# Optimization experiments

Hardware: AMD Instinct MI355X
Metric: run time of the kernel (lower is better)

The kernel has to match this reference:

```python
import jax, jax.numpy as jnp
import numpy as np

N_NODES = 50000
N_EDGES = 800000
D_IN = 256
D_OUT = 256
BN_EPS = 1e-5


def setup_inputs() -> dict:
    key = jax.random.key(0)
    ks = jax.random.split(key, 10)
    h = jax.random.normal(ks[0], (N_NODES, D_IN), dtype=jnp.float32)
    e = jax.random.uniform(ks[1], (N_EDGES, 1), dtype=jnp.float32)
    src = jax.random.randint(ks[2], (N_EDGES,), 0, N_NODES, dtype=jnp.int32)
    dst = jax.random.randint(ks[3], (N_EDGES,), 0, N_NODES, dtype=jnp.int32)
    s1 = 1.0 / np.sqrt(D_IN)
    s2 = 1.0 / np.sqrt(D_OUT)
    W1 = jax.random.uniform(ks[4], (D_OUT, D_IN), jnp.float32, -s1, s1)
    b1 = jax.random.uniform(ks[5], (D_OUT,), jnp.float32, -s1, s1)
    W2 = jax.random.uniform(ks[6], (D_OUT, D_OUT), jnp.float32, -s2, s2)
    b2 = jax.random.uniform(ks[7], (D_OUT,), jnp.float32, -s2, s2)
    gamma = jnp.ones((D_OUT,), jnp.float32)
    beta = jnp.zeros((D_OUT,), jnp.float32)
    return {"h": h, "e": e, "src": src, "dst": dst, "W1": W1, "b1": b1,
            "W2": W2, "b2": b2, "gamma": gamma, "beta": beta}


def reference(h, e, src, dst, W1, b1, W2, b2, gamma, beta):
    N = h.shape[0]
    # u_mul_e: gather source node feats, scale by per-edge weight. msg: [E, D_IN]
    msg = h[src] * e
    # mean aggregation over incoming edges per destination node
    agg = jax.ops.segment_sum(msg, dst, num_segments=N)
    deg = jax.ops.segment_sum(jnp.ones((src.shape[0],), h.dtype), dst, num_segments=N)
    hn = jnp.where(deg[:, None] > 0, agg / jnp.maximum(deg, 1.0)[:, None], 0.0)
    # 2-layer MLP with ReLU
    x = jax.nn.relu(hn @ W1.T + b1)
    x = jax.nn.relu(x @ W2.T + b2)
    # BatchNorm1d (training mode: batch statistics, biased variance)
    mu = jnp.mean(x, axis=0)
    var = jnp.var(x, axis=0)
    x = gamma * (x - mu) * jax.lax.rsqrt(var + BN_EPS) + beta
    # residual (in_feats == out_feats): add aggregated features
    return x + hn
```

## Files before the change

### kernel.cpp

```cpp
#include <hip/hip_runtime.h>

#define D 256
#define NCHUNK 512
#define MAXBKT 1024
#define EBCAP 2176

typedef __attribute__((ext_vector_type(8))) short bf16x8;
typedef __attribute__((ext_vector_type(8))) unsigned short u16x8;
typedef __attribute__((ext_vector_type(4))) float f32x4;

__device__ __forceinline__ unsigned short bfr(float x) {
    unsigned u = __float_as_uint(x);
    unsigned r = (u + 0x7fffu + ((u >> 16) & 1u)) >> 16;
    return (unsigned short)r;
}
__device__ __forceinline__ float bf2f(unsigned short u) {
    return __uint_as_float(((unsigned)u) << 16);
}
__device__ __forceinline__ void gload_lds16(const void* g, void* l) {
    __builtin_amdgcn_global_load_lds((const __attribute__((address_space(1))) unsigned int*)g,
                                     (__attribute__((address_space(3))) unsigned int*)l, 16, 0, 0);
}

__global__ void cvt_kernel(const float* __restrict__ in, unsigned short* __restrict__ out,
                           long n4, const float* __restrict__ W1, const float* __restrict__ W2,
                           unsigned short* __restrict__ w1b, unsigned short* __restrict__ w2b) {
    long stride = (long)gridDim.x * blockDim.x;
    long i0 = (long)blockIdx.x * blockDim.x + threadIdx.x;
    for (long i = i0; i < n4; i += stride) {
        float4 v = reinterpret_cast<const float4*>(in)[i];
        ushort4 o;
        o.x = bfr(v.x); o.y = bfr(v.y); o.z = bfr(v.z); o.w = bfr(v.w);
        reinterpret_cast<ushort4*>(out)[i] = o;
    }
    for (long i = i0; i < 16384; i += stride) {
        float4 a = reinterpret_cast<const float4*>(W1)[i];
        float4 b = reinterpret_cast<const float4*>(W2)[i];
        ushort4 oa, ob;
        oa.x = bfr(a.x); oa.y = bfr(a.y); oa.z = bfr(a.z); oa.w = bfr(a.w);
        ob.x = bfr(b.x); ob.y = bfr(b.y); ob.z = bfr(b.z); ob.w = bfr(b.w);
        reinterpret_cast<ushort4*>(w1b)[i] = oa;
        reinterpret_cast<ushort4*>(w2b)[i] = ob;
    }
}

__global__ void bucket_hist_kernel(const int* __restrict__ dst, int* __restrict__ cntA,
                                   int E, int EPC, int nbkt) {
    __shared__ int hist[MAXBKT];
    int c = blockIdx.x, t = threadIdx.x;
    for (int i = t; i < nbkt; i += 256) hist[i] = 0;
    __syncthreads();
    int eend = min(E, (c + 1) * EPC);
    for (int i = c * EPC + t; i < eend; i += 256) atomicAdd(&hist[dst[i] >> 6], 1);
    __syncthreads();
    for (int i = t; i < nbkt; i += 256) cntA[(size_t)c * nbkt + i] = hist[i];
}

__global__ __launch_bounds__(NCHUNK) void bucket_base_kernel(const int* __restrict__ cntA,
                                                             int* __restrict__ relbase,
                                                             int* __restrict__ btot, int nbkt) {
    int b = blockIdx.x, c = threadIdx.x;
    int v = cntA[(size_t)c * nbkt + b];
    int lane = c & 63, w = c >> 6;
    int s = v;
    for (int off = 1; off < 64; off <<= 1) {
        int u = __shfl_up(s, off, 64);
        if (lane >= off) s += u;
    }
    __shared__ int wsum[NCHUNK / 64];
    if (lane == 63) wsum[w] = s;
    __syncthreads();
    int woff = 0;
#pragma unroll
    for (int i = 0; i < NCHUNK / 64; ++i) if (i < w) woff += wsum[i];
    int incl = s + woff;
    relbase[(size_t)c * nbkt + b] = incl - v;
    if (c == NCHUNK - 1) btot[b] = incl;
}

__global__ void bucket_scatter_kernel(const int* __restrict__ src, const float* __restrict__ e,
                                      const int* __restrict__ dst, const int* __restrict__ relbase,
                                      const int* __restrict__ btot, int2* __restrict__ ev,
                                      int E, int EPC, int nbkt) {
    __shared__ int cur[MAXBKT];
    __shared__ int boff[MAXBKT];
    __shared__ int wsum[4];
    int c = blockIdx.x, t = threadIdx.x;
    {
        int base = t * 4;
        int c0 = 0, c1 = 0, c2 = 0, c3 = 0;
        if (base + 3 < nbkt) {
            int4 cc = *reinterpret_cast<const int4*>(&btot[base]);
            c0 = cc.x; c1 = cc.y; c2 = cc.z; c3 = cc.w;
        } else {
            if (base + 0 < nbkt) c0 = btot[base + 0];
            if (base + 1 < nbkt) c1 = btot[base + 1];
            if (base + 2 < nbkt) c2 = btot[base + 2];
            if (base + 3 < nbkt) c3 = btot[base + 3];
        }
        int s0 = c0, s1 = s0 + c1, s2 = s1 + c2, s3 = s2 + c3;
        int lane = t & 63, w = t >> 6;
        int v = s3;
        for (int off = 1; off < 64; off <<= 1) {
            int u = __shfl_up(v, off, 64);
            if (lane >= off) v += u;
        }
        if (lane == 63) wsum[w] = v;
        __syncthreads();
        int woff = 0;
#pragma unroll
        for (int i = 0; i < 4; ++i) if (i < w) woff += wsum[i];
        int p = woff + (v - s3);
        if (base + 0 < nbkt) boff[base + 0] = p;
        if (base + 1 < nbkt) boff[base + 1] = p + s0;
        if (base + 2 < nbkt) boff[base + 2] = p + s1;
        if (base + 3 < nbkt) boff[base + 3] = p + s2;
    }
    __syncthreads();
    for (int i = t; i < nbkt; i += 256) cur[i] = relbase[(size_t)c * nbkt + i] + boff[i];
    __syncthreads();
    int eend = min(E, (c + 1) * EPC);
    for (int i = c * EPC + t; i < eend; i += 256) {
        int d = dst[i];
        int pos = atomicAdd(&cur[d >> 6], 1);
        ev[pos] = make_int2(src[i] | ((d & 63) << 16), __float_as_int(e[i]));
    }
}

__global__ __launch_bounds__(256) void reorder_kernel(const int2* __restrict__ ev,
                                                      const int* __restrict__ btot,
                                                      int* __restrict__ offsets,
                                                      int2* __restrict__ ev2, int N, int nbkt,
                                                      int E) {
    __shared__ int2 ebr[EBCAP];
    __shared__ int2 eb2[EBCAP];
    __shared__ int cnt[64], loff[64], cur[64];
    __shared__ int wsum[4];
    __shared__ int ebeg_s;
    int b = blockIdx.x, t = threadIdx.x;
    int ns = b * 64;
    int nn = min(N, ns + 64) - ns;
    if (t < 64) { cnt[t] = 0; cur[t] = 0; }
    {
        int base = t * 4;
        int c0 = 0, c1 = 0, c2 = 0, c3 = 0;
        if (base + 3 < nbkt) {
            int4 cc = *reinterpret_cast<const int4*>(&btot[base]);
            c0 = cc.x; c1 = cc.y; c2 = cc.z; c3 = cc.w;
        } else {
            if (base + 0 < nbkt) c0 = btot[base + 0];
            if (base + 1 < nbkt) c1 = btot[base + 1];
            if (base + 2 < nbkt) c2 = btot[base + 2];
            if (base + 3 < nbkt) c3 = btot[base + 3];
        }
        int s0 = c0, s1 = s0 + c1, s2 = s1 + c2, s3 = s2 + c3;
        int lane = t & 63, w = t >> 6;
        int v = s3;
        for (int off = 1; off < 64; off <<= 1) {
            int u = __shfl_up(v, off, 64);
            if (lane >= off) v += u;
        }
        if (lane == 63) wsum[w] = v;
        __syncthreads();
        int woff = 0;
#pragma unroll
        for (int i = 0; i < 4; ++i) if (i < w) woff += wsum[i];
        int p = woff + (v - s3);
        if (b >= base && b < base + 4) {
            int pb = p;
            if (b > base + 0) pb += s0 - s0, pb = p + ((b == base + 1) ? s0 : (b == base + 2) ? s1 : s2);
            else pb = p;
            ebeg_s = pb;
        }
    }
    __syncthreads();
    int ebeg = ebeg_s;
    int ecnt = min(btot[b], EBCAP);
    for (int i = t; i < ecnt; i += 256) {
        int2 v = ev[ebeg + i];
        ebr[i] = v;
        atomicAdd(&cnt[(v.x >> 16) & 63], 1);
    }
    __syncthreads();
    if (t < 64) {
        int v = cnt[t];
        int s = v;
        for (int off = 1; off < 64; off <<= 1) {
            int u = __shfl_up(s, off, 64);
            if (t >= off) s += u;
        }
        loff[t] = s - v;
        if (t < nn) offsets[ns + t + 1] = ebeg + s;
    }
    if (b == 0 && t == 0) offsets[0] = 0;
    __syncthreads();
    for (int i = t; i < ecnt; i += 256) {
        int2 v = ebr[i];
        int nl = (v.x >> 16) & 63;
        int p = loff[nl] + atomicAdd(&cur[nl], 1);
        eb2[p] = make_int2(v.x & 0xffff, v.y);
    }
    __syncthreads();
    for (int i = t; i < ecnt; i += 256) ev2[ebeg + i] = eb2[i];
}

__global__ void aggregate_kernel(const unsigned short* __restrict__ hb, const int2* __restrict__ ev,
                                 const int* __restrict__ offsets, unsigned short* __restrict__ hnb,
                                 int n_nodes) {
    int wid = blockIdx.x * 4 + (threadIdx.x >> 6);
    if (wid >= n_nodes) return;
    int lane = threadIdx.x & 63;
    int beg = offsets[wid], end = offsets[wid + 1];
    float ax = 0.f, ay = 0.f, az = 0.f, aw = 0.f;
    int k = beg;
    for (; k + 8 <= end; k += 8) {
        int2 ee[8];
        ushort4 hh[8];
#pragma unroll
        for (int u = 0; u < 8; ++u) ee[u] = ev[k + u];
#pragma unroll
        for (int u = 0; u < 8; ++u)
            hh[u] = *reinterpret_cast<const ushort4*>(&hb[(size_t)ee[u].x * D + lane * 4]);
#pragma unroll
        for (int u = 0; u < 8; ++u) {
            float w0 = __int_as_float(ee[u].y);
            ax += bf2f(hh[u].x) * w0; ay += bf2f(hh[u].y) * w0;
            az += bf2f(hh[u].z) * w0; aw += bf2f(hh[u].w) * w0;
        }
    }
    for (; k < end; ++k) {
        int2 e0 = ev[k];
        ushort4 h0 = *reinterpret_cast<const ushort4*>(&hb[(size_t)e0.x * D + lane * 4]);
        float w0 = __int_as_float(e0.y);
        ax += bf2f(h0.x) * w0; ay += bf2f(h0.y) * w0;
        az += bf2f(h0.z) * w0; aw += bf2f(h0.w) * w0;
    }
    int deg = end - beg;
    float inv = (deg > 0) ? (1.0f / (float)deg) : 0.0f;
    ushort4 o;
    o.x = bfr(ax * inv); o.y = bfr(ay * inv); o.z = bfr(az * inv); o.w = bfr(aw * inv);
    *reinterpret_cast<ushort4*>(&hnb[(size_t)wid * D + lane * 4]) = o;
}

template <int FUSE_STATS>
__global__ __launch_bounds__(256) void gemm_kernel(const unsigned short* __restrict__ A,
                                                   const unsigned short* __restrict__ Wb,
                                                   const float* __restrict__ bias,
                                                   unsigned short* __restrict__ Cout,
                                                   float* __restrict__ partial, int P2, int M) {
    __shared__ short As[128 * 64];
    __shared__ short Bs[128 * 64];
    const int t = threadIdx.x;
    const int row0 = blockIdx.x * 128;
    const int col0 = blockIdx.y * 128;
    const int lane = t & 63;
    const int w = t >> 6;
    const int wr = (w >> 1) * 64;
    const int wc = (w & 1) * 64;
    const int lr = lane & 15;
    const int q = lane >> 4;

    f32x4 zero = {0.f, 0.f, 0.f, 0.f};
    f32x4 acc[4][4];
#pragma unroll
    for (int i = 0; i < 4; ++i)
#pragma unroll
        for (int j = 0; j < 4; ++j) acc[i][j] = zero;

    const char* Ab = reinterpret_cast<const char*>(A);
    const char* Bb = reinterpret_cast<const char*>(Wb);

#pragma unroll
    for (int kt = 0; kt < 4; ++kt) {
#pragma unroll
        for (int i = 0; i < 4; ++i) {
            int g = i * 256 + t;
            int r = g >> 3;
            int so = ((g & 7) << 4) ^ ((r & 7) << 4);
            gload_lds16(Ab + (size_t)(row0 + r) * 512 + kt * 128 + so,
                        reinterpret_cast<char*>(As) + g * 16);
        }
#pragma unroll
        for (int i = 0; i < 4; ++i) {
            int g = i * 256 + t;
            int r = g >> 3;
            int so = ((g & 7) << 4) ^ ((r & 7) << 4);
            gload_lds16(Bb + (size_t)(col0 + r) * 512 + kt * 128 + so,
                        reinterpret_cast<char*>(Bs) + g * 16);
        }
        __syncthreads();
#pragma unroll
        for (int ks = 0; ks < 2; ++ks) {
            bf16x8 a[4], b[4];
#pragma unroll
            for (int fr = 0; fr < 4; ++fr) {
                int r = wr + fr * 16 + lr;
                a[fr] = *reinterpret_cast<const bf16x8*>(
                    reinterpret_cast<const char*>(As) + r * 128 +
                    ((ks * 64 + q * 16) ^ ((r & 7) << 4)));
            }
#pragma unroll
            for (int fc = 0; fc < 4; ++fc) {
                int r = wc + fc * 16 + lr;
                b[fc] = *reinterpret_cast<const bf16x8*>(
                    reinterpret_cast<const char*>(Bs) + r * 128 +
                    ((ks * 64 + q * 16) ^ ((r & 7) << 4)));
            }
#pragma unroll
            for (int fr = 0; fr < 4; ++fr)
#pragma unroll
                for (int fc = 0; fc < 4; ++fc)
                    acc[fr][fc] = __builtin_amdgcn_mfma_f32_16x16x32_bf16(a[fr], b[fc],
                                                                          acc[fr][fc], 0, 0, 0);
        }
        if (kt < 3) __syncthreads();
    }

    float csum[4] = {0.f, 0.f, 0.f, 0.f};
    float csq[4] = {0.f, 0.f, 0.f, 0.f};
#pragma unroll
    for (int fc = 0; fc < 4; ++fc) {
        int col = col0 + wc + fc * 16 + lr;
        float bv = bias[col];
#pragma unroll
        for (int fr = 0; fr < 4; ++fr) {
#pragma unroll
            for (int rr = 0; rr < 4; ++rr) {
                int row = row0 + wr + fr * 16 + q * 4 + rr;
                if (row < M) {
                    float v = fmaxf(acc[fr][fc][rr] + bv, 0.f);
                    Cout[(size_t)row * D + col] = bfr(v);
                    if (FUSE_STATS) { csum[fc] += v; csq[fc] += v * v; }
                }
            }
        }
    }

    if (FUSE_STATS) {
#pragma unroll
        for (int fc = 0; fc < 4; ++fc) {
            float s = csum[fc], qq = csq[fc];
            s += __shfl_xor(s, 16, 64); s += __shfl_xor(s, 32, 64);
            qq += __shfl_xor(qq, 16, 64); qq += __shfl_xor(qq, 32, 64);
            if (lane < 16) {
                int col = col0 + wc + fc * 16 + lane;
                int slot = blockIdx.x * 2 + (w >> 1);
                partial[(size_t)col * P2 + slot] = s;
                partial[(size_t)(col + 256) * P2 + slot] = qq;
            }
        }
    }
}

__global__ void bn_finalize_kernel(const float* __restrict__ partial, const float* __restrict__ gamma,
                                   const float* __restrict__ beta, float* __restrict__ scaleshift,
                                   int nslots, int P2, int n) {
    int c = blockIdx.x;
    int t = threadIdx.x;
    float s = 0.f, q = 0.f;
    for (int b = t; b < nslots; b += 256) {
        s += partial[(size_t)c * P2 + b];
        q += partial[(size_t)(c + 256) * P2 + b];
    }
    int lane = t & 63, w = t >> 6;
    for (int off = 1; off < 64; off <<= 1) {
        s += __shfl_xor(s, off, 64);
        q += __shfl_xor(q, off, 64);
    }
    __shared__ float ss[4], qs[4];
    if (lane == 0) { ss[w] = s; qs[w] = q; }
    __syncthreads();
    if (t == 0) {
        float S = ss[0] + ss[1] + ss[2] + ss[3];
        float Q = qs[0] + qs[1] + qs[2] + qs[3];
        float mu = S / (float)n;
        float var = Q / (float)n - mu * mu;
        float rs = rsqrtf(var + 1e-5f);
        float sc = gamma[c] * rs;
        scaleshift[c] = sc;
        scaleshift[D + c] = beta[c] - mu * sc;
    }
}

__global__ void bn_apply_kernel(float* __restrict__ out, const unsigned short* __restrict__ x2b,
                                const unsigned short* __restrict__ hnb,
                                const float* __restrict__ scaleshift, long total4) {
    long stride = (long)gridDim.x * blockDim.x;
    for (long i = (long)blockIdx.x * blockDim.x + threadIdx.x; i < total4; i += stride) {
        int c4 = (int)(i & 63);
        ushort4 xu = reinterpret_cast<const ushort4*>(x2b)[i];
        ushort4 hu = reinterpret_cast<const ushort4*>(hnb)[i];
        float4 sc = reinterpret_cast<const float4*>(scaleshift)[c4];
        float4 sh = reinterpret_cast<const float4*>(scaleshift)[64 + c4];
        float4 v;
        v.x = bf2f(xu.x) * sc.x + sh.x + bf2f(hu.x);
        v.y = bf2f(xu.y) * sc.y + sh.y + bf2f(hu.y);
        v.z = bf2f(xu.z) * sc.z + sh.z + bf2f(hu.z);
        v.w = bf2f(xu.w) * sc.w + sh.w + bf2f(hu.w);
        reinterpret_cast<float4*>(out)[i] = v;
    }
}

extern "C" void kernel_launch(void* const* d_in, const int* in_sizes, int n_in,
                              void* d_out, int out_size, void* d_ws, size_t ws_size,
                              hipStream_t stream) {
    const float* h     = (const float*)d_in[0];
    const float* e     = (const float*)d_in[1];
    const int*   src   = (const int*)d_in[2];
    const int*   dst   = (const int*)d_in[3];
    const float* W1    = (const float*)d_in[4];
    const float* b1    = (const float*)d_in[5];
    const float* W2    = (const float*)d_in[6];
    const float* b2    = (const float*)d_in[7];
    const float* gamma = (const float*)d_in[8];
    const float* beta  = (const float*)d_in[9];
    float* out = (float*)d_out;

    const int N = in_sizes[0] / D;
    const int E = in_sizes[2];
    const size_t NB = (size_t)N * D;
    const int nrb = (N + 127) / 128;
    const int nslots = nrb * 2;
    const int P2 = (nslots + 15) & ~15;
    const int nbkt = (N + 63) / 64;
    const int EPC = (E + NCHUNK - 1) / NCHUNK;

    char* ws = (char*)d_ws;
    unsigned short* h_bf = (unsigned short*)ws; ws += NB * 2;
    unsigned short* hnb  = (unsigned short*)ws; ws += NB * 2;
    unsigned short* x1b  = (unsigned short*)ws; ws += NB * 2;
    int2* ev             = (int2*)ws;           ws += (size_t)E * 8;
    int2* ev2            = (int2*)ws;           ws += (size_t)E * 8;
    float* partial       = (float*)ws;          ws += (size_t)512 * P2 * 4;
    float* scaleshift    = (float*)ws;          ws += 2 * D * sizeof(float);
    int* offsets         = (int*)ws;            ws += (size_t)(N + 1) * 4;
    int* cntA            = (int*)ws;            ws += (size_t)NCHUNK * nbkt * 4;
    int* relbase         = (int*)ws;            ws += (size_t)NCHUNK * nbkt * 4;
    int* btot            = (int*)ws;            ws += (size_t)nbkt * 4;
    unsigned short* w1b  = (unsigned short*)ws; ws += (size_t)D * D * 2;
    unsigned short* w2b  = (unsigned short*)ws; ws += (size_t)D * D * 2;
    unsigned short* x2b  = h_bf;

    cvt_kernel<<<2048, 256, 0, stream>>>(h, h_bf, (long)(NB / 4), W1, W2, w1b, w2b);

    bucket_hist_kernel<<<NCHUNK, 256, 0, stream>>>(dst, cntA, E, EPC, nbkt);
    bucket_base_kernel<<<nbkt, NCHUNK, 0, stream>>>(cntA, relbase, btot, nbkt);
    bucket_scatter_kernel<<<NCHUNK, 256, 0, stream>>>(src, e, dst, relbase, btot, ev,
                                                      E, EPC, nbkt);
    reorder_kernel<<<nbkt, 256, 0, stream>>>(ev, btot, offsets, ev2, N, nbkt, E);

    aggregate_kernel<<<(N + 3) / 4, 256, 0, stream>>>(h_bf, ev2, offsets, hnb, N);

    dim3 ggrid(nrb, 2);
    gemm_kernel<0><<<ggrid, 256, 0, stream>>>(hnb, w1b, b1, x1b, nullptr, P2, N);
    gemm_kernel<1><<<ggrid, 256, 0, stream>>>(x1b, w2b, b2, x2b, partial, P2, N);

    bn_finalize_kernel<<<256, 256, 0, stream>>>(partial, gamma, beta, scaleshift, nslots, P2, N);
    bn_apply_kernel<<<2048, 256, 0, stream>>>(out, x2b, hnb, scaleshift, (long)(NB / 4));
}
```

Before: 189.3 us.

## Slice aggregation by feature columns and split edges across lane groups

Replaces the one-wave-per-node aggregation with a kernel where each block handles a 64-byte feature slice (8 slices per row), and within a wave 4 groups of 16 lanes process different edges in parallel, reducing with cross-lane shuffles. Adjacent blocks work on the same nodes but different column slices, so the edge list is re-read 8 times, in exchange for more parallelism per node and possibly better cache locality per slice. Each gathered access is now 64 bytes per edge per slice, and the grid is 8x larger.

New measurement: 281.4 us. 1.49x slower.

```diff
diff --git a/kernel.cpp b/kernel.cpp
--- a/kernel.cpp
+++ b/kernel.cpp
@@ -6,7 +6,6 @@
 #define EBCAP 2176
 
 typedef __attribute__((ext_vector_type(8))) short bf16x8;
-typedef __attribute__((ext_vector_type(8))) unsigned short u16x8;
 typedef __attribute__((ext_vector_type(4))) float f32x4;
 
 __device__ __forceinline__ unsigned short bfr(float x) {
@@ -168,7 +167,7 @@
         int p = woff + (v - s3);
         if (b >= base && b < base + 4) {
             int pb = p;
-            if (b > base + 0) pb += s0 - s0, pb = p + ((b == base + 1) ? s0 : (b == base + 2) ? s1 : s2);
+            if (b > base + 0) pb = p + ((b == base + 1) ? s0 : (b == base + 2) ? s1 : s2);
             else pb = p;
             ebeg_s = pb;
         }
@@ -204,42 +203,45 @@
     for (int i = t; i < ecnt; i += 256) ev2[ebeg + i] = eb2[i];
 }
 
-__global__ void aggregate_kernel(const unsigned short* __restrict__ hb, const int2* __restrict__ ev,
-                                 const int* __restrict__ offsets, unsigned short* __restrict__ hnb,
-                                 int n_nodes) {
-    int wid = blockIdx.x * 4 + (threadIdx.x >> 6);
-    if (wid >= n_nodes) return;
+__global__ __launch_bounds__(256) void aggregate_sliced_kernel(
+        const unsigned short* __restrict__ hb, const int2* __restrict__ ev,
+        const int* __restrict__ offsets, unsigned short* __restrict__ hnb, int N) {
+    int slice = blockIdx.x & 7;
+    int node = (blockIdx.x >> 3) * 4 + (threadIdx.x >> 6);
+    if (node >= N) return;
     int lane = threadIdx.x & 63;
-    int beg = offsets[wid], end = offsets[wid + 1];
-    float ax = 0.f, ay = 0.f, az = 0.f, aw = 0.f;
-    int k = beg;
-    for (; k + 8 <= end; k += 8) {
-        int2 ee[8];
-        ushort4 hh[8];
-#pragma unroll
-        for (int u = 0; u < 8; ++u) ee[u] = ev[k + u];
-#pragma unroll
-        for (int u = 0; u < 8; ++u)
-            hh[u] = *reinterpret_cast<const ushort4*>(&hb[(size_t)ee[u].x * D + lane * 4]);
-#pragma unroll
-        for (int u = 0; u < 8; ++u) {
-            float w0 = __int_as_float(ee[u].y);
-            ax += bf2f(hh[u].x) * w0; ay += bf2f(hh[u].y) * w0;
-            az += bf2f(hh[u].z) * w0; aw += bf2f(hh[u].w) * w0;
-        }
-    }
-    for (; k < end; ++k) {
+    int g = lane >> 4;
+    int l = lane & 15;
+    int beg = offsets[node], end = offsets[node + 1];
+    float a0 = 0.f, a1 = 0.f;
+    const char* base = reinterpret_cast<const char*>(hb) + slice * 64 + l * 4;
+    int k = beg + g;
+    for (; k + 4 < end; k += 8) {
         int2 e0 = ev[k];
-        ushort4 h0 = *reinterpret_cast<const ushort4*>(&hb[(size_t)e0.x * D + lane * 4]);
+        int2 e1 = ev[k + 4];
+        unsigned v0 = *reinterpret_cast<const unsigned*>(base + (size_t)e0.x * 512);
+        unsigned v1 = *reinterpret_cast<const unsigned*>(base + (size_t)e1.x * 512);
         float w0 = __int_as_float(e0.y);
-        ax += bf2f(h0.x) * w0; ay += bf2f(h0.y) * w0;
-        az += bf2f(h0.z) * w0; aw += bf2f(h0.w) * w0;
-    }
-    int deg = end - beg;
-    float inv = (deg > 0) ? (1.0f / (float)deg) : 0.0f;
-    ushort4 o;
-    o.x = bfr(ax * inv); o.y = bfr(ay * inv); o.z = bfr(az * inv); o.w = bfr(aw * inv);
-    *reinterpret_cast<ushort4*>(&hnb[(size_t)wid * D + lane * 4]) = o;
+        float w1 = __int_as_float(e1.y);
+        a0 += bf2f((unsigned short)(v0 & 0xffff)) * w0 + bf2f((unsigned short)(v1 & 0xffff)) * w1;
+        a1 += bf2f((unsigned short)(v0 >> 16)) * w0 + bf2f((unsigned short)(v1 >> 16)) * w1;
+    }
+    if (k < end) {
+        int2 e0 = ev[k];
+        unsigned v0 = *reinterpret_cast<const unsigned*>(base + (size_t)e0.x * 512);
+        float w0 = __int_as_float(e0.y);
+        a0 += bf2f((unsigned short)(v0 & 0xffff)) * w0;
+        a1 += bf2f((unsigned short)(v0 >> 16)) * w0;
+    }
+    a0 += __shfl_xor(a0, 16, 64); a0 += __shfl_xor(a0, 32, 64);
+    a1 += __shfl_xor(a1, 16, 64); a1 += __shfl_xor(a1, 32, 64);
+    if (g == 0) {
+        int deg = end - beg;
+        float inv = (deg > 0) ? (1.0f / (float)deg) : 0.0f;
+        unsigned o = (unsigned)bfr(a0 * inv) | ((unsigned)bfr(a1 * inv) << 16);
+        *reinterpret_cast<unsigned*>(reinterpret_cast<char*>(hnb) + (size_t)node * 512 +
+                                     slice * 64 + l * 4) = o;
+    }
 }
 
 template <int FUSE_STATS>
@@ -449,7 +451,8 @@
                                                       E, EPC, nbkt);
     reorder_kernel<<<nbkt, 256, 0, stream>>>(ev, btot, offsets, ev2, N, nbkt, E);
 
-    aggregate_kernel<<<(N + 3) / 4, 256, 0, stream>>>(h_bf, ev2, offsets, hnb, N);
+    int ngrp = (N + 3) / 4;
+    aggregate_sliced_kernel<<<ngrp * 8, 256, 0, stream>>>(h_bf, ev2, offsets, hnb, N);
 
     dim3 ggrid(nrb, 2);
     gemm_kernel<0><<<ggrid, 256, 0, stream>>>(hnb, w1b, b1, x1b, nullptr, P2, N);
```
